# Kernel tuning notes

Hardware: AMD Instinct MI355X
Metric: run time of the kernel (lower is better)

## Reference

```python
import jax, jax.numpy as jnp
import numpy as np

B, S, I, H, O = 2048, 128, 1, 512, 1
OUT_SEQ_LEN = 24


def setup_inputs() -> dict:
    key = jax.random.key(0)
    ks = jax.random.split(key, 12)
    s = 1.0 / np.sqrt(H)
    u = lambda k, shape: jax.random.uniform(k, shape, jnp.float32, -s, s)
    return {
        'x': jax.random.normal(ks[0], (B, S, I), jnp.float32),
        'enc_Wih': u(ks[1], (H, I)),
        'enc_Whh': u(ks[2], (H, H)),
        'enc_bih': u(ks[3], (H,)),
        'enc_bhh': u(ks[4], (H,)),
        'dec_Wih': u(ks[5], (H, I)),
        'dec_Whh': u(ks[6], (H, H)),
        'dec_bih': u(ks[7], (H,)),
        'dec_bhh': u(ks[8], (H,)),
        'fc_W': u(ks[9], (O, H)),
        'fc_b': u(ks[10], (O,)),
    }


def reference(x, enc_Wih, enc_Whh, enc_bih, enc_bhh,
              dec_Wih, dec_Whh, dec_bih, dec_bhh, fc_W, fc_b):
    batch = x.shape[0]
    h0 = jnp.zeros((batch, H), x.dtype)

    # Encoder: vanilla tanh RNN, h_t = tanh(x_t W_ih^T + b_ih + h_{t-1} W_hh^T + b_hh)
    def enc_step(h, xt):
        h2 = jnp.tanh(xt @ enc_Wih.T + enc_bih + h @ enc_Whh.T + enc_bhh)
        return h2, None

    hT, _ = jax.lax.scan(enc_step, h0, jnp.swapaxes(x, 0, 1))  # scan over S

    def dec_step(carry, _):
        h, inp = carry
        h2 = jnp.tanh(inp @ dec_Wih.T + dec_bih + h @ dec_Whh.T + dec_bhh)
        out = h2 @ fc_W.T + fc_b  # [B, O]
        return (h2, out), out

    dec_in0 = x[:, -1, :]  # [B, I]
    _, outs = jax.lax.scan(dec_step, (hT, dec_in0), None, length=OUT_SEQ_LEN)
    outputs = jnp.swapaxes(outs, 0, 1)  # [B, OUT_SEQ_LEN, O]
    return outputs[..., 0]  # squeeze(-1) since O == 1
```

## Files before the change

### kernel.cpp

```cpp
#include <hip/hip_runtime.h>
#include <math.h>

#define BATCH 2048
#define SEQ   128
#define HID   512
#define OUTT  24
#define RPB   8
#define NBLK  (BATCH/RPB)
#define TPB   1024
#define NTW   2
#define KTN   (HID/32)
#define HOLD_KT 6
#define LDSB_KT 4
#define STR_KT  (KTN - HOLD_KT - LDSB_KT)
#define LDSB_BASE HOLD_KT
#define STR_BASE  (HOLD_KT + LDSB_KT)

typedef _Float16 half8 __attribute__((ext_vector_type(8)));
typedef float   floatx4 __attribute__((ext_vector_type(4)));

__device__ __forceinline__ void mfma_hv(floatx4& c, half8 a, half8 b) {
    c = __builtin_amdgcn_mfma_f32_16x16x32_f16(a, b, c, 0, 0, 0);
}

#define PIN_AGPR(x) asm volatile("" : "+a"(x))

__device__ __forceinline__ float ftanh(float x) {
    float e = __builtin_amdgcn_exp2f(x * 2.885390081777927f);
    float r = __builtin_amdgcn_rcpf(e + 1.0f);
    return fmaf(-2.0f, r, 1.0f);
}

__global__ __launch_bounds__(256) void pack_wfrag(const float* __restrict__ W,
                                                  _Float16* __restrict__ Bw)
{
    int id   = blockIdx.x * 256 + threadIdx.x;
    int lane = id & 63;
    int nt   = (id >> 6) & 31;
    int kt   = id >> 11;
    int n  = nt * 16 + (lane & 15);
    int k0 = kt * 32 + (lane >> 4) * 8;
    const float* src = W + (size_t)n * HID + k0;
    half8 v;
    #pragma unroll
    for (int j = 0; j < 8; j++) v[j] = (_Float16)src[j];
    *(half8*)&Bw[(size_t)id * 8] = v;
}

__global__ __launch_bounds__(TPB)
__attribute__((amdgpu_waves_per_eu(4, 4)))
void rnn_persist(
    const float* __restrict__ x,
    const _Float16* __restrict__ BwE,
    const _Float16* __restrict__ BwD,
    const float* __restrict__ encWih, const float* __restrict__ encBih,
    const float* __restrict__ encBhh,
    const float* __restrict__ decWih, const float* __restrict__ decBih,
    const float* __restrict__ decBhh,
    const float* __restrict__ fcW, const float* __restrict__ fcB,
    float* __restrict__ out)
{
    __shared__ _Float16 A[KTN * 512];
    __shared__ _Float16 BwL[LDSB_KT * 16384];
    __shared__ float    xs[RPB][SEQ];
    __shared__ float    cWi[2][HID];
    __shared__ float    cBb[2][HID];
    __shared__ float    dec_in_s[RPB];

    const int tid  = threadIdx.x;
    const int lane = tid & 63;
    const int wv   = tid >> 6;
    const int row0 = blockIdx.x * RPB;
    const int c    = lane & 15;
    const int q    = lane >> 4;
    const int qh   = q & 1;
    const int lohalf = q >> 1;
    const int mB   = qh * 4;

    const float fcb0 = fcB[0];

    if (tid < HID) {
        cWi[0][tid] = encWih[tid];
        cBb[0][tid] = encBih[tid] + encBhh[tid];
        cWi[1][tid] = decWih[tid];
        cBb[1][tid] = decBih[tid] + decBhh[tid];
    }

    {
        const float4* xg = (const float4*)(x + (size_t)row0 * SEQ);
        if (tid < RPB * SEQ / 4) ((float4*)xs)[tid] = xg[tid];
    }

    for (int i = tid; i < KTN * 512 / 2; i += TPB) ((int*)A)[i] = 0;

    {
        const float4* src = (const float4*)(BwE + (size_t)LDSB_BASE * 16384);
        float4* dst = (float4*)BwL;
        #pragma unroll
        for (int i = 0; i < LDSB_KT * 16384 / 8 / TPB; i++)
            dst[i * TPB + tid] = src[i * TPB + tid];
    }

    const int    ldsAoff = q * 128 + ((c ^ q) << 3);
    const size_t bbase   = (size_t)(wv * NTW) * 512 + (size_t)lane * 8;
    const int    bbL     = wv * NTW * 512 + lane * 8;

    half8 wreg[HOLD_KT][NTW];
    #pragma unroll
    for (int kt = 0; kt < HOLD_KT; kt++)
        #pragma unroll
        for (int i = 0; i < NTW; i++) {
            wreg[kt][i] = *(const half8*)&BwE[bbase + (size_t)kt * 16384 + i * 512];
            PIN_AGPR(wreg[kt][i]);
        }

    __syncthreads();

    for (int t = 0; t < SEQ + OUTT; t++) {
        const bool enc = (t < SEQ);
        const _Float16* __restrict__ Bw = enc ? BwE : BwD;

        if (t == SEQ) {
            #pragma unroll
            for (int kt = 0; kt < HOLD_KT; kt++)
                #pragma unroll
                for (int i = 0; i < NTW; i++) {
                    wreg[kt][i] = *(const half8*)&BwD[bbase + (size_t)kt * 16384 + i * 512];
                    PIN_AGPR(wreg[kt][i]);
                }
            const float4* src = (const float4*)(BwD + (size_t)LDSB_BASE * 16384);
            float4* dst = (float4*)BwL;
            #pragma unroll
            for (int i = 0; i < LDSB_KT * 16384 / 8 / TPB; i++)
                dst[i * TPB + tid] = src[i * TPB + tid];
            __syncthreads();
        }

        floatx4 acc[NTW];
        #pragma unroll
        for (int i = 0; i < NTW; i++) acc[i] = (floatx4){0.f, 0.f, 0.f, 0.f};

        half8 bcur[NTW], bnxt[NTW];
        #pragma unroll
        for (int i = 0; i < NTW; i++) {
            bcur[i] = *(const half8*)&Bw[bbase + (size_t)STR_BASE * 16384 + i * 512];
            bnxt[i] = *(const half8*)&Bw[bbase + (size_t)(STR_BASE + 1) * 16384 + i * 512];
        }

        #pragma unroll
        for (int kt = 0; kt < HOLD_KT; kt++) {
            half8 a = *(const half8*)&A[kt * 512 + ldsAoff];
            #pragma unroll
            for (int i = 0; i < NTW; i++)
                mfma_hv(acc[i], a, wreg[kt][i]);
        }

        #pragma unroll
        for (int kl = 0; kl < LDSB_KT; kl++) {
            half8 a = *(const half8*)&A[(LDSB_BASE + kl) * 512 + ldsAoff];
            #pragma unroll
            for (int i = 0; i < NTW; i++) {
                half8 b = *(const half8*)&BwL[kl * 16384 + bbL + i * 512];
                mfma_hv(acc[i], a, b);
            }
        }

        #pragma unroll
        for (int s = 0; s < STR_KT; s++) {
            const int kt = STR_BASE + s;
            half8 bpre[NTW];
            if (s + 2 < STR_KT) {
                #pragma unroll
                for (int i = 0; i < NTW; i++)
                    bpre[i] = *(const half8*)&Bw[bbase + (size_t)(kt + 2) * 16384 + i * 512];
            }
            half8 a = *(const half8*)&A[kt * 512 + ldsAoff];
            #pragma unroll
            for (int i = 0; i < NTW; i++)
                mfma_hv(acc[i], a, bcur[i]);
            #pragma unroll
            for (int i = 0; i < NTW; i++) {
                bcur[i] = bnxt[i];
                if (s + 2 < STR_KT) bnxt[i] = bpre[i];
            }
        }

        __syncthreads();

        float inp[4];
        if (enc) {
            #pragma unroll
            for (int r = 0; r < 4; r++) inp[r] = xs[mB + r][t];
        } else if (t == SEQ) {
            #pragma unroll
            for (int r = 0; r < 4; r++) inp[r] = xs[mB + r][SEQ - 1];
        } else {
            #pragma unroll
            for (int r = 0; r < 4; r++) inp[r] = dec_in_s[mB + r];
        }

        const int sel = enc ? 0 : 1;
        #pragma unroll
        for (int i = 0; i < NTW; i++) {
            int n = (wv * NTW + i) * 16 + c;
            int G = (n >> 3) & 3;
            int base = (n >> 5) * 512 + G * 128 + (n & 7);
            float wi = cWi[sel][n];
            float bb = cBb[sel][n];
            #pragma unroll
            for (int r = 0; r < 4; r++) {
                float sum = acc[i][r] + __shfl_xor(acc[i][r], 32, 64);
                float v = ftanh(sum + inp[r] * wi + bb);
                _Float16 hh = (_Float16)v;
                _Float16 rs = (_Float16)(v - (float)hh);
                int mw = mB + r + (lohalf << 3);
                A[base + ((mw ^ G) << 3)] = lohalf ? rs : hh;
            }
        }
        __syncthreads();

        if (!enc) {
            if (wv < 8) {
                const int m = wv;
                float sfc = 0.f;
                #pragma unroll
                for (int ii = 0; ii < HID / 64; ii++) {
                    int k = ii * 64 + lane;
                    int G = (k >> 3) & 3;
                    int a0 = (k >> 5) * 512 + G * 128 + (k & 7);
                    float hv = (float)A[a0 + ((m ^ G) << 3)]
                             + (float)A[a0 + (((m + 8) ^ G) << 3)];
                    sfc = fmaf(hv, fcW[k], sfc);
                }
                #pragma unroll
                for (int off = 32; off > 0; off >>= 1)
                    sfc += __shfl_down(sfc, off, 64);
                if (lane == 0) {
                    float o = sfc + fcb0;
                    dec_in_s[m] = o;
                    out[(size_t)(row0 + m) * OUTT + (t - SEQ)] = o;
                }
            }
            __syncthreads();
        }
    }
}

extern "C" void kernel_launch(void* const* d_in, const int* in_sizes, int n_in,
                              void* d_out, int out_size, void* d_ws, size_t ws_size,
                              hipStream_t stream)
{
    const float* x        = (const float*)d_in[0];
    const float* enc_Wih  = (const float*)d_in[1];
    const float* enc_Whh  = (const float*)d_in[2];
    const float* enc_bih  = (const float*)d_in[3];
    const float* enc_bhh  = (const float*)d_in[4];
    const float* dec_Wih  = (const float*)d_in[5];
    const float* dec_Whh  = (const float*)d_in[6];
    const float* dec_bih  = (const float*)d_in[7];
    const float* dec_bhh  = (const float*)d_in[8];
    const float* fc_W     = (const float*)d_in[9];
    const float* fc_b     = (const float*)d_in[10];
    float* out = (float*)d_out;

    const size_t wfrag = (size_t)HID * HID;
    _Float16* BwE = (_Float16*)d_ws;
    _Float16* BwD = BwE + wfrag;

    pack_wfrag<<<HID * HID / (256 * 8), 256, 0, stream>>>(enc_Whh, BwE);
    pack_wfrag<<<HID * HID / (256 * 8), 256, 0, stream>>>(dec_Whh, BwD);

    rnn_persist<<<NBLK, TPB, 0, stream>>>(
        x, BwE, BwD,
        enc_Wih, enc_bih, enc_bhh,
        dec_Wih, dec_bih, dec_bhh,
        fc_W, fc_b, out);
}
```

Measured before the change: 617.7 us.

## Process 16 batch rows per block using separate hi/lo A tiles

Doubles the rows per block from 8 to 16. The hi and lo fp16 halves of the hidden state are stored in two separate LDS tiles, so all 16 M rows of each MFMA carry real batch rows, and each weight fragment now feeds two MFMAs (hi and lo accumulators). This halves the number of blocks and the total weight traffic per batch row. In exchange it drops the register-pinned weight fragments and shrinks the LDS-resident weight slice from 4 to 3 k-tiles to make room for the larger A tiles. More of the weights must therefore be streamed from global or L2 on every timestep, and each block does twice as much work per step on the serial critical path.

```diff
diff --git a/kernel.cpp b/kernel.cpp
--- a/kernel.cpp
+++ b/kernel.cpp
@@ -5,16 +5,16 @@
 #define SEQ   128
 #define HID   512
 #define OUTT  24
-#define RPB   8
+#define RPB   16
 #define NBLK  (BATCH/RPB)
 #define TPB   1024
 #define NTW   2
 #define KTN   (HID/32)
-#define HOLD_KT 6
-#define LDSB_KT 4
-#define STR_KT  (KTN - HOLD_KT - LDSB_KT)
-#define LDSB_BASE HOLD_KT
-#define STR_BASE  (HOLD_KT + LDSB_KT)
+#define LDSB_KT 3
+#define STR_KT  (KTN - LDSB_KT)
+#define LDSB_BASE 0
+#define STR_BASE  LDSB_KT
+#define ATILE 8192
 
 typedef _Float16 half8 __attribute__((ext_vector_type(8)));
 typedef float   floatx4 __attribute__((ext_vector_type(4)));
@@ -22,8 +22,6 @@
 __device__ __forceinline__ void mfma_hv(floatx4& c, half8 a, half8 b) {
     c = __builtin_amdgcn_mfma_f32_16x16x32_f16(a, b, c, 0, 0, 0);
 }
-
-#define PIN_AGPR(x) asm volatile("" : "+a"(x))
 
 __device__ __forceinline__ float ftanh(float x) {
     float e = __builtin_amdgcn_exp2f(x * 2.885390081777927f);
@@ -60,7 +58,7 @@
     const float* __restrict__ fcW, const float* __restrict__ fcB,
     float* __restrict__ out)
 {
-    __shared__ _Float16 A[KTN * 512];
+    __shared__ _Float16 A[2 * ATILE];
     __shared__ _Float16 BwL[LDSB_KT * 16384];
     __shared__ float    xs[RPB][SEQ];
     __shared__ float    cWi[2][HID];
@@ -73,9 +71,7 @@
     const int row0 = blockIdx.x * RPB;
     const int c    = lane & 15;
     const int q    = lane >> 4;
-    const int qh   = q & 1;
-    const int lohalf = q >> 1;
-    const int mB   = qh * 4;
+    const int mB   = q * 4;
 
     const float fcb0 = fcB[0];
 
@@ -91,7 +87,7 @@
         if (tid < RPB * SEQ / 4) ((float4*)xs)[tid] = xg[tid];
     }
 
-    for (int i = tid; i < KTN * 512 / 2; i += TPB) ((int*)A)[i] = 0;
+    for (int i = tid; i < 2 * ATILE / 2; i += TPB) ((int*)A)[i] = 0;
 
     {
         const float4* src = (const float4*)(BwE + (size_t)LDSB_BASE * 16384);
@@ -105,15 +101,6 @@
     const size_t bbase   = (size_t)(wv * NTW) * 512 + (size_t)lane * 8;
     const int    bbL     = wv * NTW * 512 + lane * 8;
 
-    half8 wreg[HOLD_KT][NTW];
-    #pragma unroll
-    for (int kt = 0; kt < HOLD_KT; kt++)
-        #pragma unroll
-        for (int i = 0; i < NTW; i++) {
-            wreg[kt][i] = *(const half8*)&BwE[bbase + (size_t)kt * 16384 + i * 512];
-            PIN_AGPR(wreg[kt][i]);
-        }
-
     __syncthreads();
 
     for (int t = 0; t < SEQ + OUTT; t++) {
@@ -121,13 +108,6 @@
         const _Float16* __restrict__ Bw = enc ? BwE : BwD;
 
         if (t == SEQ) {
-            #pragma unroll
-            for (int kt = 0; kt < HOLD_KT; kt++)
-                #pragma unroll
-                for (int i = 0; i < NTW; i++) {
-                    wreg[kt][i] = *(const half8*)&BwD[bbase + (size_t)kt * 16384 + i * 512];
-                    PIN_AGPR(wreg[kt][i]);
-                }
             const float4* src = (const float4*)(BwD + (size_t)LDSB_BASE * 16384);
             float4* dst = (float4*)BwL;
             #pragma unroll
@@ -136,9 +116,12 @@
             __syncthreads();
         }
 
-        floatx4 acc[NTW];
-        #pragma unroll
-        for (int i = 0; i < NTW; i++) acc[i] = (floatx4){0.f, 0.f, 0.f, 0.f};
+        floatx4 accH[NTW], accL[NTW];
+        #pragma unroll
+        for (int i = 0; i < NTW; i++) {
+            accH[i] = (floatx4){0.f, 0.f, 0.f, 0.f};
+            accL[i] = (floatx4){0.f, 0.f, 0.f, 0.f};
+        }
 
         half8 bcur[NTW], bnxt[NTW];
         #pragma unroll
@@ -148,20 +131,14 @@
         }
 
         #pragma unroll
-        for (int kt = 0; kt < HOLD_KT; kt++) {
-            half8 a = *(const half8*)&A[kt * 512 + ldsAoff];
-            #pragma unroll
-            for (int i = 0; i < NTW; i++)
-                mfma_hv(acc[i], a, wreg[kt][i]);
-        }
-
-        #pragma unroll
         for (int kl = 0; kl < LDSB_KT; kl++) {
-            half8 a = *(const half8*)&A[(LDSB_BASE + kl) * 512 + ldsAoff];
+            half8 ah = *(const half8*)&A[(LDSB_BASE + kl) * 512 + ldsAoff];
+            half8 al = *(const half8*)&A[ATILE + (LDSB_BASE + kl) * 512 + ldsAoff];
             #pragma unroll
             for (int i = 0; i < NTW; i++) {
                 half8 b = *(const half8*)&BwL[kl * 16384 + bbL + i * 512];
-                mfma_hv(acc[i], a, b);
+                mfma_hv(accH[i], ah, b);
+                mfma_hv(accL[i], al, b);
             }
         }
 
@@ -174,10 +151,13 @@
                 for (int i = 0; i < NTW; i++)
                     bpre[i] = *(const half8*)&Bw[bbase + (size_t)(kt + 2) * 16384 + i * 512];
             }
-            half8 a = *(const half8*)&A[kt * 512 + ldsAoff];
-            #pragma unroll
-            for (int i = 0; i < NTW; i++)
-                mfma_hv(acc[i], a, bcur[i]);
+            half8 ah = *(const half8*)&A[kt * 512 + ldsAoff];
+            half8 al = *(const half8*)&A[ATILE + kt * 512 + ldsAoff];
+            #pragma unroll
+            for (int i = 0; i < NTW; i++) {
+                mfma_hv(accH[i], ah, bcur[i]);
+                mfma_hv(accL[i], al, bcur[i]);
+            }
             #pragma unroll
             for (int i = 0; i < NTW; i++) {
                 bcur[i] = bnxt[i];
@@ -209,37 +189,35 @@
             float bb = cBb[sel][n];
             #pragma unroll
             for (int r = 0; r < 4; r++) {
-                float sum = acc[i][r] + __shfl_xor(acc[i][r], 32, 64);
-                float v = ftanh(sum + inp[r] * wi + bb);
+                int m = mB + r;
+                float v = ftanh(accH[i][r] + accL[i][r] + inp[r] * wi + bb);
                 _Float16 hh = (_Float16)v;
                 _Float16 rs = (_Float16)(v - (float)hh);
-                int mw = mB + r + (lohalf << 3);
-                A[base + ((mw ^ G) << 3)] = lohalf ? rs : hh;
+                int off = base + ((m ^ G) << 3);
+                A[off]         = hh;
+                A[ATILE + off] = rs;
             }
         }
         __syncthreads();
 
         if (!enc) {
-            if (wv < 8) {
-                const int m = wv;
-                float sfc = 0.f;
-                #pragma unroll
-                for (int ii = 0; ii < HID / 64; ii++) {
-                    int k = ii * 64 + lane;
-                    int G = (k >> 3) & 3;
-                    int a0 = (k >> 5) * 512 + G * 128 + (k & 7);
-                    float hv = (float)A[a0 + ((m ^ G) << 3)]
-                             + (float)A[a0 + (((m + 8) ^ G) << 3)];
-                    sfc = fmaf(hv, fcW[k], sfc);
-                }
-                #pragma unroll
-                for (int off = 32; off > 0; off >>= 1)
-                    sfc += __shfl_down(sfc, off, 64);
-                if (lane == 0) {
-                    float o = sfc + fcb0;
-                    dec_in_s[m] = o;
-                    out[(size_t)(row0 + m) * OUTT + (t - SEQ)] = o;
-                }
+            const int m = wv;
+            float sfc = 0.f;
+            #pragma unroll
+            for (int ii = 0; ii < HID / 64; ii++) {
+                int k = ii * 64 + lane;
+                int G = (k >> 3) & 3;
+                int a0 = (k >> 5) * 512 + G * 128 + (k & 7) + ((m ^ G) << 3);
+                float hv = (float)A[a0] + (float)A[ATILE + a0];
+                sfc = fmaf(hv, fcW[k], sfc);
+            }
+            #pragma unroll
+            for (int off = 32; off > 0; off >>= 1)
+                sfc += __shfl_down(sfc, off, 64);
+            if (lane == 0) {
+                float o = sfc + fcb0;
+                dec_in_s[m] = o;
+                out[(size_t)(row0 + m) * OUTT + (t - SEQ)] = o;
             }
             __syncthreads();
         }
```

New measurement: 764.8 us. +23.8%, slower.
